# Performance work log

Measured on AMD Instinct MI355X. Metric: run time of the kernel, lower is better.

The kernel has to match this reference:

```python
import jax, jax.numpy as jnp
import numpy as np

D_MODEL = 1024
NUM_HEADS = 16
HEAD_DIM = D_MODEL // NUM_HEADS
B, T = 4, 2048


def setup_inputs() -> dict:
    key = jax.random.key(0)
    ks = jax.random.split(key, 6)
    s = 1.0 / np.sqrt(D_MODEL)  # ~ nn.Linear init scale
    return {
        "x_q": jax.random.normal(ks[0], (B, T, D_MODEL), jnp.float32),
        "x_kv": jax.random.normal(ks[1], (B, T, D_MODEL), jnp.float32),
        "Wq": jax.random.uniform(ks[2], (D_MODEL, D_MODEL), jnp.float32, -s, s),
        "Wk": jax.random.uniform(ks[3], (D_MODEL, D_MODEL), jnp.float32, -s, s),
        "Wv": jax.random.uniform(ks[4], (D_MODEL, D_MODEL), jnp.float32, -s, s),
        "Wo": jax.random.uniform(ks[5], (D_MODEL, D_MODEL), jnp.float32, -s, s),
    }


def reference(x_q, x_kv, Wq, Wk, Wv, Wo):
    Bq, Tq, C = x_q.shape
    Tk = x_kv.shape[1]
    # torch nn.Linear: y = x @ W.T
    q = (x_q @ Wq.T).reshape(Bq, Tq, NUM_HEADS, HEAD_DIM).transpose(0, 2, 1, 3)
    k = (x_kv @ Wk.T).reshape(Bq, Tk, NUM_HEADS, HEAD_DIM).transpose(0, 2, 1, 3)
    v = (x_kv @ Wv.T).reshape(Bq, Tk, NUM_HEADS, HEAD_DIM).transpose(0, 2, 1, 3)
    scores = jnp.einsum("bhqd,bhkd->bhqk", q, k) / jnp.sqrt(
        jnp.asarray(HEAD_DIM, x_q.dtype)
    )
    causal = jnp.triu(jnp.ones((Tq, Tk), bool), k=1)  # True above diagonal
    scores = jnp.where(causal, -jnp.inf, scores)
    attn = jax.nn.softmax(scores, axis=-1)
    out = jnp.einsum("bhqk,bhkd->bhqd", attn, v)
    out = out.transpose(0, 2, 1, 3).reshape(Bq, Tq, C)
    return out @ Wo.T
```

## Files before the change

kernel.cpp:

```cpp
#include <hip/hip_runtime.h>
#include <stdint.h>

#define T_SEQ 2048
#define NH 16
#define HD 64
#define DM 1024
#define BB 4
#define MROWS (BB * T_SEQ)

typedef __attribute__((ext_vector_type(8))) __bf16 bf16x8;
typedef __attribute__((ext_vector_type(8))) unsigned short u16x8;
typedef __attribute__((ext_vector_type(4))) unsigned short u16x4;
typedef __attribute__((ext_vector_type(4))) float f32x4;

__device__ __forceinline__ unsigned short f2bf(float f) {
  unsigned int x = __float_as_uint(f);
  x = (x + 0x7fffu + ((x >> 16) & 1u)) >> 16;
  return (unsigned short)x;
}

__device__ __forceinline__ bf16x8 ld8_f32(const float* __restrict__ p) {
  f32x4 a = *(const f32x4*)p;
  f32x4 b = *(const f32x4*)(p + 4);
  u16x8 u;
#pragma unroll
  for (int i = 0; i < 4; ++i) {
    u[i]     = f2bf(a[i]);
    u[i + 4] = f2bf(b[i]);
  }
  return __builtin_bit_cast(bf16x8, u);
}

__device__ __forceinline__ bf16x8 ld8_bf(const unsigned short* p) {
  return __builtin_bit_cast(bf16x8, *(const u16x8*)p);
}

__device__ __forceinline__ bf16x8 ld8_lds(const unsigned short* p) {
  u16x4 a = *(const u16x4*)p;
  u16x4 b = *(const u16x4*)(p + 4);
  return __builtin_bit_cast(bf16x8,
      __builtin_shufflevector(a, b, 0, 1, 2, 3, 4, 5, 6, 7));
}

__device__ __forceinline__ u16x4 lo4(u16x8 v) {
  return __builtin_shufflevector(v, v, 0, 1, 2, 3);
}
__device__ __forceinline__ u16x4 hi4(u16x8 v) {
  return __builtin_shufflevector(v, v, 4, 5, 6, 7);
}

__device__ __forceinline__ void gload_lds16(const unsigned short* g,
                                            unsigned short* l) {
  __builtin_amdgcn_global_load_lds(
      (const __attribute__((address_space(1))) unsigned int*)g,
      (__attribute__((address_space(3))) unsigned int*)l, 16, 0, 0);
}

__global__ __launch_bounds__(256) void conv_f32_bf16(
    const float* __restrict__ src, unsigned short* __restrict__ dst, int n8) {
  const int i = blockIdx.x * 256 + threadIdx.x;
  if (i < n8)
    *(u16x8*)(dst + (size_t)i * 8) =
        __builtin_bit_cast(u16x8, ld8_f32(src + (size_t)i * 8));
}

__global__ __launch_bounds__(256) void conv_w4(
    const float* __restrict__ s0, const float* __restrict__ s1,
    const float* __restrict__ s2, const float* __restrict__ s3,
    unsigned short* __restrict__ d012, unsigned short* __restrict__ d3,
    int n8) {
  const int y = blockIdx.y;
  const float* src = (y == 0) ? s0 : (y == 1) ? s1 : (y == 2) ? s2 : s3;
  unsigned short* dst = (y < 3) ? d012 + (size_t)y * DM * DM : d3;
  const int i = blockIdx.x * 256 + threadIdx.x;
  if (i < n8)
    *(u16x8*)(dst + (size_t)i * 8) =
        __builtin_bit_cast(u16x8, ld8_f32(src + (size_t)i * 8));
}

template <int MODE>
__global__ __launch_bounds__(256) void gemm128(
    const unsigned short* __restrict__ A, const unsigned short* __restrict__ B,
    void* __restrict__ Cv, int M, int N, int K) {
  __shared__ __align__(16) unsigned short As[128 * 32];
  __shared__ __align__(16) unsigned short Bs[128 * 32];

  const int t = threadIdx.x;
  const int lane = t & 63, wave = t >> 6;
  const int m0 = blockIdx.y * 128, n0 = blockIdx.x * 128;

  const int srow = t >> 2;
  const int scol = (t & 3) * 8;
  const unsigned short* ga0 = A + (size_t)(m0 + srow) * K + scol;
  const unsigned short* ga1 = A + (size_t)(m0 + 64 + srow) * K + scol;
  const unsigned short* gb0 = B + (size_t)(n0 + srow) * K + scol;
  const unsigned short* gb1 = B + (size_t)(n0 + 64 + srow) * K + scol;
  unsigned short* lA0 = &As[(wave * 16) * 32];
  unsigned short* lA1 = &As[(64 + wave * 16) * 32];
  unsigned short* lB0 = &Bs[(wave * 16) * 32];
  unsigned short* lB1 = &Bs[(64 + wave * 16) * 32];

  const int mw = (wave >> 1) * 64, nw = (wave & 1) * 64;
  const int fr = lane & 15, fq = (lane >> 4) * 8;

  f32x4 acc[4][4];
#pragma unroll
  for (int i = 0; i < 4; ++i)
#pragma unroll
    for (int j = 0; j < 4; ++j) acc[i][j] = (f32x4){0.f, 0.f, 0.f, 0.f};

  for (int k0 = 0; k0 < K; k0 += 32) {
    __syncthreads();
    gload_lds16(ga0 + k0, lA0);
    gload_lds16(ga1 + k0, lA1);
    gload_lds16(gb0 + k0, lB0);
    gload_lds16(gb1 + k0, lB1);
    __syncthreads();

    bf16x8 af[4], bfr[4];
#pragma unroll
    for (int i = 0; i < 4; ++i)
      af[i] = ld8_bf(&As[(mw + i * 16 + fr) * 32 + fq]);
#pragma unroll
    for (int j = 0; j < 4; ++j)
      bfr[j] = ld8_bf(&Bs[(nw + j * 16 + fr) * 32 + fq]);
#pragma unroll
    for (int i = 0; i < 4; ++i)
#pragma unroll
      for (int j = 0; j < 4; ++j)
        acc[i][j] = __builtin_amdgcn_mfma_f32_16x16x32_bf16(af[i], bfr[j],
                                                            acc[i][j], 0, 0, 0);
  }

  const int orow = (lane >> 4) * 4, ocol = lane & 15;
#pragma unroll
  for (int i = 0; i < 4; ++i)
#pragma unroll
    for (int j = 0; j < 4; ++j) {
      if constexpr (MODE == 2) {
        const int mb = m0 + mw + i * 16 + orow;
        const int n = n0 + nw + j * 16 + ocol;
        u16x4 pk;
#pragma unroll
        for (int r = 0; r < 4; ++r) pk[r] = f2bf(acc[i][j][r]);
        unsigned short* dst = (unsigned short*)Cv +
            ((size_t)((mb >> 11) * NH + (n >> 6)) * HD + (n & 63)) * T_SEQ +
            (mb & 2047);
        *(u16x4*)dst = pk;
      } else {
#pragma unroll
        for (int r = 0; r < 4; ++r) {
          const size_t idx = (size_t)(m0 + mw + i * 16 + orow + r) * N +
                             (n0 + nw + j * 16 + ocol);
          if constexpr (MODE == 1)
            ((float*)Cv)[idx] = acc[i][j][r];
          else
            ((unsigned short*)Cv)[idx] = f2bf(acc[i][j][r]);
        }
      }
    }
}

#define ASTR 68

__global__ __launch_bounds__(256, 2) void attn_flash2(
    const unsigned short* Qw, const unsigned short* __restrict__ Kw,
    const unsigned short* __restrict__ Vt, unsigned short* Ow) {
  __shared__ __align__(16) unsigned short k_lds[64][ASTR];
  __shared__ __align__(16) unsigned short vt_lds[64][ASTR];
  __shared__ __align__(16) unsigned short p_lds[4][32][ASTR];
  __shared__ float alpha_lds[4][32];
  __shared__ float l_lds[4][32];

  const int tid = threadIdx.x, lane = tid & 63, wave = tid >> 6;
  const int c16 = lane & 15, quad = lane >> 4;
  const int b = blockIdx.z, h = blockIdx.y;
  const int pi = blockIdx.x;
  const int qb0A = (15 - pi) * 128;
  const int qb0B = pi * 128;
  const size_t rkbase = (size_t)b * T_SEQ * DM + (size_t)h * HD;
  const size_t vtbase = (size_t)(b * NH + h) * HD * T_SEQ;

  const int q_loA = qb0A + wave * 32;
  const int q_loB = qb0B + wave * 32;

  bf16x8 qfA[2][2], qfB[2][2];
#pragma unroll
  for (int nf = 0; nf < 2; ++nf) {
    const unsigned short* qpA =
        Qw + rkbase + (size_t)(q_loA + nf * 16 + c16) * DM + quad * 8;
    qfA[nf][0] = ld8_bf(qpA);
    qfA[nf][1] = ld8_bf(qpA + 32);
    const unsigned short* qpB =
        Qw + rkbase + (size_t)(q_loB + nf * 16 + c16) * DM + quad * 8;
    qfB[nf][0] = ld8_bf(qpB);
    qfB[nf][1] = ld8_bf(qpB + 32);
  }

  f32x4 oA[2][4], oB[2][4];
#pragma unroll
  for (int nf = 0; nf < 2; ++nf)
#pragma unroll
    for (int j = 0; j < 4; ++j) {
      oA[nf][j] = (f32x4){0.f, 0.f, 0.f, 0.f};
      oB[nf][j] = (f32x4){0.f, 0.f, 0.f, 0.f};
    }
  float mA[2] = {-3.0e38f, -3.0e38f}, lA[2] = {0.f, 0.f};
  float mB[2] = {-3.0e38f, -3.0e38f}, lB[2] = {0.f, 0.f};

  const int srow = tid >> 2;
  const int scol = (tid & 3) * 16;
  const int ntiles = (qb0A + 191) >> 6;
  const int ntA_w = (q_loA + 95) >> 6;
  const int ntB_w = (q_loB + 95) >> 6;

  const unsigned short* kp0 = Kw + rkbase + (size_t)srow * DM + scol;
  const unsigned short* vp0 = Vt + vtbase + (size_t)srow * T_SEQ + scol;

  auto subtile = [&](const bf16x8 (&qf)[2][2], f32x4 (&o)[2][4],
                     float (&m_r)[2], float (&l_r)[2], const int q_lo,
                     const int kb0) {
    f32x4 s[4][2];
    __builtin_amdgcn_s_setprio(1);
#pragma unroll
    for (int mf = 0; mf < 4; ++mf) {
      const unsigned short* kr = &k_lds[mf * 16 + c16][quad * 8];
      const bf16x8 k0 = ld8_lds(kr);
      const bf16x8 k1 = ld8_lds(kr + 32);
#pragma unroll
      for (int nf = 0; nf < 2; ++nf) {
        f32x4 a = {0.f, 0.f, 0.f, 0.f};
        a = __builtin_amdgcn_mfma_f32_16x16x32_bf16(k0, qf[nf][0], a, 0, 0, 0);
        a = __builtin_amdgcn_mfma_f32_16x16x32_bf16(k1, qf[nf][1], a, 0, 0, 0);
        s[mf][nf] = a;
      }
    }
    __builtin_amdgcn_s_setprio(0);
    if (kb0 + 63 > q_lo) {
#pragma unroll
      for (int mf = 0; mf < 4; ++mf) {
        const int key0 = kb0 + mf * 16 + quad * 4;
#pragma unroll
        for (int nf = 0; nf < 2; ++nf) {
          const int qg = q_lo + nf * 16 + c16;
#pragma unroll
          for (int r = 0; r < 4; ++r)
            s[mf][nf][r] =
                (key0 + r <= qg) ? s[mf][nf][r] * 0.125f : -3.0e38f;
        }
      }
    } else {
#pragma unroll
      for (int mf = 0; mf < 4; ++mf)
#pragma unroll
        for (int nf = 0; nf < 2; ++nf)
#pragma unroll
          for (int r = 0; r < 4; ++r) s[mf][nf][r] *= 0.125f;
    }

#pragma unroll
    for (int nf = 0; nf < 2; ++nf) {
      float mx = -3.0e38f;
#pragma unroll
      for (int mf = 0; mf < 4; ++mf)
#pragma unroll
        for (int r = 0; r < 4; ++r) mx = fmaxf(mx, s[mf][nf][r]);
      mx = fmaxf(mx, __shfl_xor(mx, 16, 64));
      mx = fmaxf(mx, __shfl_xor(mx, 32, 64));
      const float m_new = fmaxf(m_r[nf], mx);
      const float al = __expf(m_r[nf] - m_new);
      m_r[nf] = m_new;
      float ps = 0.f;
#pragma unroll
      for (int mf = 0; mf < 4; ++mf) {
        u16x4 pk;
#pragma unroll
        for (int r = 0; r < 4; ++r) {
          const float e = __expf(s[mf][nf][r] - m_new);
          ps += e;
          pk[r] = f2bf(e);
        }
        *(u16x4*)&p_lds[wave][nf * 16 + c16][mf * 16 + quad * 4] = pk;
      }
      ps += __shfl_xor(ps, 16, 64);
      ps += __shfl_xor(ps, 32, 64);
      l_r[nf] = l_r[nf] * al + ps;
      if (quad == 0) alpha_lds[wave][nf * 16 + c16] = al;
    }
    __threadfence_block();

#pragma unroll
    for (int nf = 0; nf < 2; ++nf) {
      float alr[4];
#pragma unroll
      for (int r = 0; r < 4; ++r)
        alr[r] = alpha_lds[wave][nf * 16 + quad * 4 + r];
#pragma unroll
      for (int j = 0; j < 4; ++j)
#pragma unroll
        for (int r = 0; r < 4; ++r) o[nf][j][r] *= alr[r];
    }

    bf16x8 pf[2][2];
#pragma unroll
    for (int nf = 0; nf < 2; ++nf) {
      const unsigned short* pw = &p_lds[wave][nf * 16 + c16][quad * 8];
      pf[nf][0] = ld8_lds(pw);
      pf[nf][1] = ld8_lds(pw + 32);
    }
    __builtin_amdgcn_s_setprio(1);
#pragma unroll
    for (int j = 0; j < 4; ++j) {
      const unsigned short* vr = &vt_lds[j * 16 + c16][quad * 8];
      const bf16x8 v0 = ld8_lds(vr);
      const bf16x8 v1 = ld8_lds(vr + 32);
#pragma unroll
      for (int nf = 0; nf < 2; ++nf) {
        o[nf][j] = __builtin_amdgcn_mfma_f32_16x16x32_bf16(pf[nf][0], v0,
                                                           o[nf][j], 0, 0, 0);
        o[nf][j] = __builtin_amdgcn_mfma_f32_16x16x32_bf16(pf[nf][1], v1,
                                                           o[nf][j], 0, 0, 0);
      }
    }
    __builtin_amdgcn_s_setprio(0);
  };

  for (int t = 0; t < ntiles; ++t) {
    const int kb0 = t * 64;
    __syncthreads();
    {
      const unsigned short* kp = kp0 + (size_t)kb0 * DM;
      u16x8 ka = *(const u16x8*)kp;
      u16x8 kc = *(const u16x8*)(kp + 8);
      const unsigned short* vp = vp0 + kb0;
      u16x8 va = *(const u16x8*)vp;
      u16x8 vc = *(const u16x8*)(vp + 8);
      *(u16x4*)&k_lds[srow][scol]       = lo4(ka);
      *(u16x4*)&k_lds[srow][scol + 4]   = hi4(ka);
      *(u16x4*)&k_lds[srow][scol + 8]   = lo4(kc);
      *(u16x4*)&k_lds[srow][scol + 12]  = hi4(kc);
      *(u16x4*)&vt_lds[srow][scol]      = lo4(va);
      *(u16x4*)&vt_lds[srow][scol + 4]  = hi4(va);
      *(u16x4*)&vt_lds[srow][scol + 8]  = lo4(vc);
      *(u16x4*)&vt_lds[srow][scol + 12] = hi4(vc);
    }
    __syncthreads();
    if (t < ntA_w) subtile(qfA, oA, mA, lA, q_loA, kb0);
    if (t < ntB_w) subtile(qfB, oB, mB, lB, q_loB, kb0);
  }

  auto epi = [&](f32x4 (&o)[2][4], float (&l_r)[2], const int q_lo) {
    if (quad == 0) {
      l_lds[wave][c16] = l_r[0];
      l_lds[wave][16 + c16] = l_r[1];
    }
    __threadfence_block();
#pragma unroll
    for (int nf = 0; nf < 2; ++nf)
#pragma unroll
      for (int r = 0; r < 4; ++r) {
        const int qg = q_lo + nf * 16 + quad * 4 + r;
        const float inv = 1.0f / l_lds[wave][nf * 16 + quad * 4 + r];
        unsigned short* orow = Ow + rkbase + (size_t)qg * DM;
#pragma unroll
        for (int j = 0; j < 4; ++j)
          orow[j * 16 + c16] = f2bf(o[nf][j][r] * inv);
      }
  };
  epi(oA, lA, q_loA);
  __threadfence_block();
  epi(oB, lB, q_loB);
}

extern "C" void kernel_launch(void* const* d_in, const int* in_sizes, int n_in,
                              void* d_out, int out_size, void* d_ws, size_t ws_size,
                              hipStream_t stream) {
  const float* x_q  = (const float*)d_in[0];
  const float* x_kv = (const float*)d_in[1];
  const float* Wq   = (const float*)d_in[2];
  const float* Wk   = (const float*)d_in[3];
  const float* Wv   = (const float*)d_in[4];
  const float* Wo   = (const float*)d_in[5];
  float* out = (float*)d_out;

  unsigned short* scr  = (unsigned short*)d_out;
  unsigned short* Sx   = scr;
  unsigned short* Wk_b = scr + (size_t)MROWS * DM;
  unsigned short* Wv_b = Wk_b + (size_t)DM * DM;
  unsigned short* Wq_b = Wv_b + (size_t)DM * DM;

  unsigned short* qb   = (unsigned short*)d_ws;
  unsigned short* kb   = qb + (size_t)MROWS * DM;
  unsigned short* vtb  = kb + (size_t)MROWS * DM;
  unsigned short* Wo_b = vtb + (size_t)MROWS * DM;

  const int nW8 = DM * DM / 8;
  const int nX8 = MROWS * DM / 8;

  conv_w4<<<dim3(nW8 / 256, 4), 256, 0, stream>>>(Wk, Wv, Wq, Wo, Wk_b, Wo_b,
                                                  nW8);
  conv_f32_bf16<<<nX8 / 256, 256, 0, stream>>>(x_kv, Sx, nX8);

  dim3 gg(DM / 128, MROWS / 128);
  gemm128<0><<<gg, 256, 0, stream>>>(Sx, Wk_b, kb, MROWS, DM, DM);
  gemm128<2><<<gg, 256, 0, stream>>>(Sx, Wv_b, vtb, MROWS, DM, DM);
  conv_f32_bf16<<<nX8 / 256, 256, 0, stream>>>(x_q, Sx, nX8);
  gemm128<0><<<gg, 256, 0, stream>>>(Sx, Wq_b, qb, MROWS, DM, DM);
  attn_flash2<<<dim3(8, NH, BB), 256, 0, stream>>>(qb, kb, vtb, qb);
  gemm128<1><<<gg, 256, 0, stream>>>(qb, Wo_b, out, MROWS, DM, DM);
}
```

Before: 335.0 us.

## Double-buffer K/V tiles in attention and deepen GEMM K-step per barrier

The attention kernel now keeps two LDS buffers for K and V^T. It issues global loads for the next tile before computing on the current one, then writes them to the alternate buffer afterwards, which removes one barrier per iteration and overlaps memory latency with MFMA work. The GEMM loads two 32-wide K slices per barrier pair into separate LDS halves, halving the number of synchronisations. Both changes raise LDS use and register pressure, which could lower occupancy. A single barrier per iteration in the attention loop relies on the ping-pong buffers to avoid overwriting data another wave is still reading.

```diff
diff --git a/kernel.cpp b/kernel.cpp
--- a/kernel.cpp
+++ b/kernel.cpp
@@ -82,8 +82,8 @@
 __global__ __launch_bounds__(256) void gemm128(
     const unsigned short* __restrict__ A, const unsigned short* __restrict__ B,
     void* __restrict__ Cv, int M, int N, int K) {
-  __shared__ __align__(16) unsigned short As[128 * 32];
-  __shared__ __align__(16) unsigned short Bs[128 * 32];
+  __shared__ __align__(16) unsigned short As[2][128 * 32];
+  __shared__ __align__(16) unsigned short Bs[2][128 * 32];
 
   const int t = threadIdx.x;
   const int lane = t & 63, wave = t >> 6;
@@ -95,10 +95,7 @@
   const unsigned short* ga1 = A + (size_t)(m0 + 64 + srow) * K + scol;
   const unsigned short* gb0 = B + (size_t)(n0 + srow) * K + scol;
   const unsigned short* gb1 = B + (size_t)(n0 + 64 + srow) * K + scol;
-  unsigned short* lA0 = &As[(wave * 16) * 32];
-  unsigned short* lA1 = &As[(64 + wave * 16) * 32];
-  unsigned short* lB0 = &Bs[(wave * 16) * 32];
-  unsigned short* lB1 = &Bs[(64 + wave * 16) * 32];
+  const int lo0 = (wave * 16) * 32, lo1 = (64 + wave * 16) * 32;
 
   const int mw = (wave >> 1) * 64, nw = (wave & 1) * 64;
   const int fr = lane & 15, fq = (lane >> 4) * 8;
@@ -109,27 +106,34 @@
 #pragma unroll
     for (int j = 0; j < 4; ++j) acc[i][j] = (f32x4){0.f, 0.f, 0.f, 0.f};
 
-  for (int k0 = 0; k0 < K; k0 += 32) {
+  for (int k0 = 0; k0 < K; k0 += 64) {
     __syncthreads();
-    gload_lds16(ga0 + k0, lA0);
-    gload_lds16(ga1 + k0, lA1);
-    gload_lds16(gb0 + k0, lB0);
-    gload_lds16(gb1 + k0, lB1);
+    gload_lds16(ga0 + k0, &As[0][lo0]);
+    gload_lds16(ga1 + k0, &As[0][lo1]);
+    gload_lds16(gb0 + k0, &Bs[0][lo0]);
+    gload_lds16(gb1 + k0, &Bs[0][lo1]);
+    gload_lds16(ga0 + k0 + 32, &As[1][lo0]);
+    gload_lds16(ga1 + k0 + 32, &As[1][lo1]);
+    gload_lds16(gb0 + k0 + 32, &Bs[1][lo0]);
+    gload_lds16(gb1 + k0 + 32, &Bs[1][lo1]);
     __syncthreads();
 
-    bf16x8 af[4], bfr[4];
-#pragma unroll
-    for (int i = 0; i < 4; ++i)
-      af[i] = ld8_bf(&As[(mw + i * 16 + fr) * 32 + fq]);
-#pragma unroll
-    for (int j = 0; j < 4; ++j)
-      bfr[j] = ld8_bf(&Bs[(nw + j * 16 + fr) * 32 + fq]);
-#pragma unroll
-    for (int i = 0; i < 4; ++i)
+#pragma unroll
+    for (int ks = 0; ks < 2; ++ks) {
+      bf16x8 af[4], bfr[4];
+#pragma unroll
+      for (int i = 0; i < 4; ++i)
+        af[i] = ld8_bf(&As[ks][(mw + i * 16 + fr) * 32 + fq]);
 #pragma unroll
       for (int j = 0; j < 4; ++j)
-        acc[i][j] = __builtin_amdgcn_mfma_f32_16x16x32_bf16(af[i], bfr[j],
-                                                            acc[i][j], 0, 0, 0);
+        bfr[j] = ld8_bf(&Bs[ks][(nw + j * 16 + fr) * 32 + fq]);
+#pragma unroll
+      for (int i = 0; i < 4; ++i)
+#pragma unroll
+        for (int j = 0; j < 4; ++j)
+          acc[i][j] = __builtin_amdgcn_mfma_f32_16x16x32_bf16(
+              af[i], bfr[j], acc[i][j], 0, 0, 0);
+    }
   }
 
   const int orow = (lane >> 4) * 4, ocol = lane & 15;
@@ -166,8 +170,8 @@
 __global__ __launch_bounds__(256, 2) void attn_flash2(
     const unsigned short* Qw, const unsigned short* __restrict__ Kw,
     const unsigned short* __restrict__ Vt, unsigned short* Ow) {
-  __shared__ __align__(16) unsigned short k_lds[64][ASTR];
-  __shared__ __align__(16) unsigned short vt_lds[64][ASTR];
+  __shared__ __align__(16) unsigned short k_lds[2][64][ASTR];
+  __shared__ __align__(16) unsigned short vt_lds[2][64][ASTR];
   __shared__ __align__(16) unsigned short p_lds[4][32][ASTR];
   __shared__ float alpha_lds[4][32];
   __shared__ float l_lds[4][32];
@@ -219,12 +223,12 @@
 
   auto subtile = [&](const bf16x8 (&qf)[2][2], f32x4 (&o)[2][4],
                      float (&m_r)[2], float (&l_r)[2], const int q_lo,
-                     const int kb0) {
+                     const int kb0, const int bi) {
     f32x4 s[4][2];
     __builtin_amdgcn_s_setprio(1);
 #pragma unroll
     for (int mf = 0; mf < 4; ++mf) {
-      const unsigned short* kr = &k_lds[mf * 16 + c16][quad * 8];
+      const unsigned short* kr = &k_lds[bi][mf * 16 + c16][quad * 8];
       const bf16x8 k0 = ld8_lds(kr);
       const bf16x8 k1 = ld8_lds(kr + 32);
 #pragma unroll
@@ -311,7 +315,7 @@
     __builtin_amdgcn_s_setprio(1);
 #pragma unroll
     for (int j = 0; j < 4; ++j) {
-      const unsigned short* vr = &vt_lds[j * 16 + c16][quad * 8];
+      const unsigned short* vr = &vt_lds[bi][j * 16 + c16][quad * 8];
       const bf16x8 v0 = ld8_lds(vr);
       const bf16x8 v1 = ld8_lds(vr + 32);
 #pragma unroll
@@ -325,28 +329,50 @@
     __builtin_amdgcn_s_setprio(0);
   };
 
+  {
+    u16x8 ka = *(const u16x8*)kp0;
+    u16x8 kc = *(const u16x8*)(kp0 + 8);
+    u16x8 va = *(const u16x8*)vp0;
+    u16x8 vc = *(const u16x8*)(vp0 + 8);
+    *(u16x4*)&k_lds[0][srow][scol]       = lo4(ka);
+    *(u16x4*)&k_lds[0][srow][scol + 4]   = hi4(ka);
+    *(u16x4*)&k_lds[0][srow][scol + 8]   = lo4(kc);
+    *(u16x4*)&k_lds[0][srow][scol + 12]  = hi4(kc);
+    *(u16x4*)&vt_lds[0][srow][scol]      = lo4(va);
+    *(u16x4*)&vt_lds[0][srow][scol + 4]  = hi4(va);
+    *(u16x4*)&vt_lds[0][srow][scol + 8]  = lo4(vc);
+    *(u16x4*)&vt_lds[0][srow][scol + 12] = hi4(vc);
+  }
+  __syncthreads();
+
+  int cur = 0;
   for (int t = 0; t < ntiles; ++t) {
     const int kb0 = t * 64;
-    __syncthreads();
-    {
-      const unsigned short* kp = kp0 + (size_t)kb0 * DM;
-      u16x8 ka = *(const u16x8*)kp;
-      u16x8 kc = *(const u16x8*)(kp + 8);
-      const unsigned short* vp = vp0 + kb0;
-      u16x8 va = *(const u16x8*)vp;
-      u16x8 vc = *(const u16x8*)(vp + 8);
-      *(u16x4*)&k_lds[srow][scol]       = lo4(ka);
-      *(u16x4*)&k_lds[srow][scol + 4]   = hi4(ka);
-      *(u16x4*)&k_lds[srow][scol + 8]   = lo4(kc);
-      *(u16x4*)&k_lds[srow][scol + 12]  = hi4(kc);
-      *(u16x4*)&vt_lds[srow][scol]      = lo4(va);
-      *(u16x4*)&vt_lds[srow][scol + 4]  = hi4(va);
-      *(u16x4*)&vt_lds[srow][scol + 8]  = lo4(vc);
-      *(u16x4*)&vt_lds[srow][scol + 12] = hi4(vc);
-    }
-    __syncthreads();
-    if (t < ntA_w) subtile(qfA, oA, mA, lA, q_loA, kb0);
-    if (t < ntB_w) subtile(qfB, oB, mB, lB, q_loB, kb0);
+    const bool pf = (t + 1 < ntiles);
+    u16x8 ka, kc, va, vc;
+    if (pf) {
+      const unsigned short* kp = kp0 + (size_t)(kb0 + 64) * DM;
+      ka = *(const u16x8*)kp;
+      kc = *(const u16x8*)(kp + 8);
+      const unsigned short* vp = vp0 + (kb0 + 64);
+      va = *(const u16x8*)vp;
+      vc = *(const u16x8*)(vp + 8);
+    }
+    if (t < ntA_w) subtile(qfA, oA, mA, lA, q_loA, kb0, cur);
+    if (t < ntB_w) subtile(qfB, oB, mB, lB, q_loB, kb0, cur);
+    if (pf) {
+      const int nb = cur ^ 1;
+      *(u16x4*)&k_lds[nb][srow][scol]       = lo4(ka);
+      *(u16x4*)&k_lds[nb][srow][scol + 4]   = hi4(ka);
+      *(u16x4*)&k_lds[nb][srow][scol + 8]   = lo4(kc);
+      *(u16x4*)&k_lds[nb][srow][scol + 12]  = hi4(kc);
+      *(u16x4*)&vt_lds[nb][srow][scol]      = lo4(va);
+      *(u16x4*)&vt_lds[nb][srow][scol + 4]  = hi4(va);
+      *(u16x4*)&vt_lds[nb][srow][scol + 8]  = lo4(vc);
+      *(u16x4*)&vt_lds[nb][srow][scol + 12] = hi4(vc);
+      __syncthreads();
+      cur = nb;
+    }
   }
 
   auto epi = [&](f32x4 (&o)[2][4], float (&l_r)[2], const int q_lo) {
```

Measured after the change: 317.4 us. -5.3%, faster.
